# Performance work log

Hardware: AMD Instinct MI355X
Metric: run time of the kernel (lower is better)

Reference implementation:

```python
import jax, jax.numpy as jnp
import numpy as np
import math

B, N, F0, HID, OUT, K = 8, 2048, 128, 64, 16, 10


def setup_inputs() -> dict:
    key = jax.random.key(0)
    ks = jax.random.split(key, 6)
    X = jax.random.normal(ks[0], (B, N, F0), dtype=jnp.float32)
    # Row-stochastic dense 'rescaled Laplacian': spectrum inside unit disk,
    # so K-th order Bernstein polynomial stays numerically stable.
    A = jax.random.uniform(ks[1], (N, N), dtype=jnp.float32)
    L = A / jnp.sum(A, axis=1, keepdims=True)
    W1 = jax.random.normal(ks[2], (F0, HID), dtype=jnp.float32) / np.float32(np.sqrt(F0))
    b1 = jnp.zeros((HID,), dtype=jnp.float32)
    W2 = jax.random.normal(ks[3], (HID, OUT), dtype=jnp.float32) / np.float32(np.sqrt(HID))
    b2 = jnp.zeros((OUT,), dtype=jnp.float32)
    theta = 0.02 * jax.random.normal(ks[4], (K + 1,), dtype=jnp.float32)
    return {"X": X, "L": L, "W1": W1, "b1": b1, "W2": W2, "b2": b2,
            "theta": theta, "dp": 0}


def _bern_filter(Hf, L, theta, binom):
    # g(L) Hf = sum_i theta_i C(K,i) L^i (I-L)^{K-i} Hf
    # Computed by applying L / (I-L) directly to the (B,N,F) features
    # (mathematically identical to forming the NxN basis matrices).
    Lap = lambda Y: jnp.einsum('vw,bwf->bvf', L, Y)
    ys = [Hf]                       # ys[k] = (I-L)^k Hf
    for _ in range(K):
        ys.append(ys[-1] - Lap(ys[-1]))
    a = theta * binom               # (K+1,)
    # Horner in L: r = a_K Hf; r <- L r + a_i (I-L)^{K-i} Hf
    r = a[K] * Hf
    for i in range(K - 1, -1, -1):
        r = Lap(r) + a[i] * ys[K - i]
    return r


def reference(X, L, W1, b1, W2, b2, theta, dp):
    binom = jnp.asarray([math.comb(K, i) for i in range(K + 1)], dtype=X.dtype)
    # dropout with p=dp=0 is identity
    Hf = jax.nn.relu(X @ W1 + b1)          # (B, N, HID)
    Hf = _bern_filter(Hf, L, theta, binom) # (B, N, HID)
    Hg = jnp.mean(Hf, axis=1)              # (B, HID)
    logits = Hg @ W2 + b2                  # (B, OUT)
    return logits
```

## Files before the change

kernel.cpp:

```cpp
#include <hip/hip_runtime.h>

#define NN     2048
#define F0D    128
#define HIDD   64
#define OUTD   16
#define KDEG   10
#define NCHAIN 128
#define COLS   16

typedef unsigned int u32;

#define CTAG(j) (0xC0DE0000u + (u32)(j))
#define HTAG    0xBEEF0001u

static __device__ __forceinline__ u32 ld_flag(const u32* p) {
    return __hip_atomic_load(p, __ATOMIC_RELAXED, __HIP_MEMORY_SCOPE_AGENT);
}
static __device__ __forceinline__ void st_flag(u32* p, u32 v) {
    __hip_atomic_store(p, v, __ATOMIC_RELAXED, __HIP_MEMORY_SCOPE_AGENT);
}
static __device__ __forceinline__ void st_data(float* p, float v) {
    __hip_atomic_store(p, v, __ATOMIC_RELAXED, __HIP_MEMORY_SCOPE_AGENT);
}

__global__ __launch_bounds__(256, 1) void k_fused(
    const float* __restrict__ X, const float* __restrict__ L,
    const float* __restrict__ W1, const float* __restrict__ b1,
    const float* __restrict__ W2, const float* __restrict__ b2,
    const float* __restrict__ theta, float* __restrict__ out,
    float* __restrict__ ws)
{
    float* PB  = ws;
    u32*   FLC = (u32*)(ws + 28672);
    u32*   FLH = (u32*)(ws + 49152);
    float* Hg  = ws + 49280;

    __shared__ union {
        struct { float Lt[NN * COLS]; float redf[4][16]; float cbv[16]; int rdy[16]; } mv;
        struct { float W1t[64][132]; float redm[16][65]; float wv[64]; } hd;
    } sm;

    const int g = blockIdx.x;
    const int t = threadIdx.x;

    if (g < NCHAIN) {
        const int u0 = g * COLS;

        if (t <= KDEG) {
            const float C10[11] = {1,10,45,120,210,252,210,120,45,10,1};
            float acc = 0.f;
            for (int i = 0; i <= t; ++i) {
                int n = KDEG - i, r = t - i;
                long long cm = 1;
                for (int s = 1; s <= r; ++s) cm = cm * (n - r + s) / s;
                float term = theta[i] * C10[i] * (float)cm;
                if ((t - i) & 1) term = -term;
                acc += term;
            }
            sm.mv.cbv[t] = acc;
        }
        if (t < 16) sm.mv.rdy[t] = 0;

        const float4* L4  = (const float4*)L;
        float4*       Lt4 = (float4*)sm.mv.Lt;
        const int qc = t & 3, r0 = t >> 2;
        {
            float4 acc = make_float4(0.f, 0.f, 0.f, 0.f);
            #pragma unroll 8
            for (int i = 0; i < 32; ++i) {
                int v = r0 + 64 * i;
                float4 lv = L4[(size_t)v * (NN / 4) + (u0 >> 2) + qc];
                Lt4[v * 4 + qc] = lv;
                acc.x += lv.x; acc.y += lv.y; acc.z += lv.z; acc.w += lv.w;
            }
            #pragma unroll
            for (int m = 4; m <= 32; m <<= 1) {
                acc.x += __shfl_xor(acc.x, m); acc.y += __shfl_xor(acc.y, m);
                acc.z += __shfl_xor(acc.z, m); acc.w += __shfl_xor(acc.w, m);
            }
            int lane = t & 63, wid = t >> 6;
            if (lane < 4) *(float4*)&sm.mv.redf[wid][lane * 4] = acc;
        }
        __syncthreads();

        float val = 0.f, wacc = 0.f;
        if (t < COLS) {
            float s = sm.mv.redf[0][t] + sm.mv.redf[1][t]
                    + sm.mv.redf[2][t] + sm.mv.redf[3][t];
            val = s; wacc = sm.mv.cbv[0];
            st_data(&PB[u0 + t], s);
        }
        if (t < 64) {
            asm volatile("s_waitcnt vmcnt(0)" ::: "memory");
            if (t == 0) st_flag(FLC + g, CTAG(1));
        }

        for (int j = 2; j <= KDEG; ++j) {
            if (t < 64) {
                const u32* fb = FLC + (size_t)(j - 2) * 128;
                const u32 tag = CTAG(j - 1);
                while (!__all(ld_flag(fb + t) == tag && ld_flag(fb + t + 64) == tag))
                    __builtin_amdgcn_s_sleep(1);
                asm volatile("" ::: "memory");
                if (t == 0) ((volatile int*)sm.mv.rdy)[j] = 1;
            } else {
                volatile int* vr = (volatile int*)sm.mv.rdy;
                while (vr[j] == 0) __builtin_amdgcn_s_sleep(1);
                asm volatile("" ::: "memory");
            }

            const float* psrc = PB + (size_t)(j - 2) * 2048;
            float xv[32];
            #pragma unroll
            for (int k = 0; k < 32; ++k) xv[k] = psrc[r0 + 64 * k];

            float4 a2 = make_float4(0.f, 0.f, 0.f, 0.f);
            #pragma unroll
            for (int k = 0; k < 32; ++k) {
                float4 lv = Lt4[(r0 + 64 * k) * 4 + qc];
                a2.x += lv.x * xv[k]; a2.y += lv.y * xv[k];
                a2.z += lv.z * xv[k]; a2.w += lv.w * xv[k];
            }
            #pragma unroll
            for (int m = 4; m <= 32; m <<= 1) {
                a2.x += __shfl_xor(a2.x, m); a2.y += __shfl_xor(a2.y, m);
                a2.z += __shfl_xor(a2.z, m); a2.w += __shfl_xor(a2.w, m);
            }
            {
                int lane = t & 63, wid = t >> 6;
                if (lane < 4) *(float4*)&sm.mv.redf[wid][lane * 4] = a2;
            }
            __syncthreads();

            if (t < COLS) {
                float s = sm.mv.redf[0][t] + sm.mv.redf[1][t]
                        + sm.mv.redf[2][t] + sm.mv.redf[3][t];
                wacc += sm.mv.cbv[j - 1] * val;
                val = s;
                float outv = (j < KDEG) ? s : (wacc + sm.mv.cbv[KDEG] * s);
                st_data(&PB[(size_t)(j - 1) * 2048 + u0 + t], outv);
            }
            if (t < 64) {
                asm volatile("s_waitcnt vmcnt(0)" ::: "memory");
                if (t == 0) st_flag(FLC + (size_t)(j - 1) * 128 + g, CTAG(j));
            }
        }

        if (g == 0) {
            if (t < 64) {
                for (;;) {
                    int ok = (ld_flag(FLH + t) == HTAG)
                           & (ld_flag(FLH + t + 64) == HTAG);
                    if (__all(ok)) break;
                    __builtin_amdgcn_s_sleep(2);
                }
                asm volatile("" ::: "memory");
            }
            __syncthreads();
            if (t < 128) {
                int o = t & 15, bb = t >> 4;
                float a3 = b2[o];
                #pragma unroll
                for (int h = 0; h < HIDD; ++h)
                    a3 += Hg[bb * 64 + h] * W2[h * 16 + o];
                out[bb * 16 + o] = a3;
            }
        }
        return;
    }

    const int u = g - NCHAIN;
    const int vchunk = u & 31, bA = u >> 5, bB = bA + 4;

    if (t == 0) {
        while (ld_flag(FLC + u) != CTAG(1)) __builtin_amdgcn_s_sleep(2);
    }
    __syncthreads();

    for (int i = t; i < F0D * HIDD; i += 256) {
        int f = i >> 6, h = i & 63;
        sm.hd.W1t[h][f] = W1[i];
    }
    __syncthreads();

    const int hg = t & 15, vg = t >> 4;
    const int vbase = vchunk * 64 + vg * 4;
    const float* XA = X + ((size_t)bA * NN + vbase) * F0D;
    const float* XB = X + ((size_t)bB * NN + vbase) * F0D;
    float accA[4][4] = {}, accB[4][4] = {};
    for (int f = 0; f < F0D; f += 4) {
        float4 xa[4], xb[4];
        #pragma unroll
        for (int i = 0; i < 4; ++i) {
            xa[i] = *(const float4*)(XA + (size_t)i * F0D + f);
            xb[i] = *(const float4*)(XB + (size_t)i * F0D + f);
        }
        #pragma unroll
        for (int jj = 0; jj < 4; ++jj) {
            float4 wr = *(const float4*)(&sm.hd.W1t[hg + 16 * jj][f]);
            #pragma unroll
            for (int i = 0; i < 4; ++i) {
                accA[i][jj] += xa[i].x * wr.x + xa[i].y * wr.y
                             + xa[i].z * wr.z + xa[i].w * wr.w;
                accB[i][jj] += xb[i].x * wr.x + xb[i].y * wr.y
                             + xb[i].z * wr.z + xb[i].w * wr.w;
            }
        }
    }

    if (t < 4) {
        const u32* fp = FLC + (size_t)(KDEG - 1) * 128 + vchunk * 4 + t;
        while (ld_flag(fp) != CTAG(KDEG)) __builtin_amdgcn_s_sleep(2);
        asm volatile("" ::: "memory");
    }
    __syncthreads();
    if (t < 16)
        ((float4*)sm.hd.wv)[t] =
            ((const float4*)(PB + (size_t)(KDEG - 1) * 2048 + vchunk * 64))[t];
    __syncthreads();

    const float inv = 1.0f / (float)NN;
    float hsA[4] = {0.f,0.f,0.f,0.f}, hsB[4] = {0.f,0.f,0.f,0.f};
    #pragma unroll
    for (int i = 0; i < 4; ++i) {
        float we = sm.hd.wv[vg * 4 + i];
        #pragma unroll
        for (int jj = 0; jj < 4; ++jj) {
            float rA = accA[i][jj] + b1[hg + 16 * jj];
            float rB = accB[i][jj] + b1[hg + 16 * jj];
            rA = rA > 0.f ? rA : 0.f;
            rB = rB > 0.f ? rB : 0.f;
            hsA[jj] += rA * we;
            hsB[jj] += rB * we;
        }
    }
    #pragma unroll
    for (int jj = 0; jj < 4; ++jj) sm.hd.redm[vg][hg + 16 * jj] = hsA[jj];
    __syncthreads();
    if (t < 64) {
        float s = 0.f;
        #pragma unroll
        for (int i = 0; i < 16; ++i) s += sm.hd.redm[i][t];
        atomicAdd(&Hg[bA * 64 + t], s * inv);
    }
    __syncthreads();
    #pragma unroll
    for (int jj = 0; jj < 4; ++jj) sm.hd.redm[vg][hg + 16 * jj] = hsB[jj];
    __syncthreads();
    if (t < 64) {
        float s = 0.f;
        #pragma unroll
        for (int i = 0; i < 16; ++i) s += sm.hd.redm[i][t];
        atomicAdd(&Hg[bB * 64 + t], s * inv);
        asm volatile("s_waitcnt vmcnt(0)" ::: "memory");
        if (t == 0) st_flag(FLH + u, HTAG);
    }
}

extern "C" void kernel_launch(void* const* d_in, const int* in_sizes, int n_in,
                              void* d_out, int out_size, void* d_ws, size_t ws_size,
                              hipStream_t stream) {
    const float* X     = (const float*)d_in[0];
    const float* L     = (const float*)d_in[1];
    const float* W1    = (const float*)d_in[2];
    const float* b1    = (const float*)d_in[3];
    const float* W2    = (const float*)d_in[4];
    const float* b2    = (const float*)d_in[5];
    const float* theta = (const float*)d_in[6];
    float* outp = (float*)d_out;
    float* wsp  = (float*)d_ws;

    hipMemsetAsync((char*)d_ws + 49152 * sizeof(float), 0, 2560, stream);

    hipLaunchKernelGGL(k_fused, dim3(256), dim3(256), 0, stream,
                       X, L, W1, b1, W2, b2, theta, outp, wsp);
}
```

Measured before the change: 132.3 us.

## Pad chain flags, double-buffer reductions, and fold W2 projection into head blocks

Each completion flag now sits on its own 64-byte slot to avoid false sharing while many blocks poll. The reduction scratch is double-buffered by step parity, and a second wavefront does the polling. The final step that waited on all head blocks is removed: each head block projects its partial mean through W2 and atomically adds into the zero-initialised output. This removes a serial global wait and an extra pass at the end, but float atomic adds make the summation order nondeterministic.

Result: faster. 118.1 us (-10.8%).

```diff
diff --git a/kernel.cpp b/kernel.cpp
--- a/kernel.cpp
+++ b/kernel.cpp
@@ -11,7 +11,6 @@
 typedef unsigned int u32;
 
 #define CTAG(j) (0xC0DE0000u + (u32)(j))
-#define HTAG    0xBEEF0001u
 
 static __device__ __forceinline__ u32 ld_flag(const u32* p) {
     return __hip_atomic_load(p, __ATOMIC_RELAXED, __HIP_MEMORY_SCOPE_AGENT);
@@ -32,11 +31,10 @@
 {
     float* PB  = ws;
     u32*   FLC = (u32*)(ws + 28672);
-    u32*   FLH = (u32*)(ws + 49152);
-    float* Hg  = ws + 49280;
 
     __shared__ union {
-        struct { float Lt[NN * COLS]; float redf[4][16]; float cbv[16]; int rdy[16]; } mv;
+        struct { float Lt[NN * COLS]; float redf[2][4][16];
+                 float cbv[16]; int rdy[16]; } mv;
         struct { float W1t[64][132]; float redm[16][65]; float wv[64]; } hd;
     } sm;
 
@@ -79,31 +77,35 @@
                 acc.z += __shfl_xor(acc.z, m); acc.w += __shfl_xor(acc.w, m);
             }
             int lane = t & 63, wid = t >> 6;
-            if (lane < 4) *(float4*)&sm.mv.redf[wid][lane * 4] = acc;
+            if (lane < 4) *(float4*)&sm.mv.redf[1][wid][lane * 4] = acc;
         }
         __syncthreads();
 
         float val = 0.f, wacc = 0.f;
         if (t < COLS) {
-            float s = sm.mv.redf[0][t] + sm.mv.redf[1][t]
-                    + sm.mv.redf[2][t] + sm.mv.redf[3][t];
+            float s = sm.mv.redf[1][0][t] + sm.mv.redf[1][1][t]
+                    + sm.mv.redf[1][2][t] + sm.mv.redf[1][3][t];
             val = s; wacc = sm.mv.cbv[0];
             st_data(&PB[u0 + t], s);
         }
         if (t < 64) {
             asm volatile("s_waitcnt vmcnt(0)" ::: "memory");
-            if (t == 0) st_flag(FLC + g, CTAG(1));
+            if (t == 0) st_flag(FLC + g * 16, CTAG(1));
         }
 
         for (int j = 2; j <= KDEG; ++j) {
-            if (t < 64) {
-                const u32* fb = FLC + (size_t)(j - 2) * 128;
+            const int par = j & 1;
+            if ((t >> 6) == 1) {
+                const u32* fb = FLC + (size_t)(j - 2) * 128 * 16;
                 const u32 tag = CTAG(j - 1);
-                while (!__all(ld_flag(fb + t) == tag && ld_flag(fb + t + 64) == tag))
+                const int l = t & 63;
+                while (!__all(ld_flag(fb + l * 16) == tag &&
+                              ld_flag(fb + (l + 64) * 16) == tag))
                     __builtin_amdgcn_s_sleep(1);
                 asm volatile("" ::: "memory");
-                if (t == 0) ((volatile int*)sm.mv.rdy)[j] = 1;
-            } else {
+                if (t == 64) ((volatile int*)sm.mv.rdy)[j] = 1;
+            }
+            {
                 volatile int* vr = (volatile int*)sm.mv.rdy;
                 while (vr[j] == 0) __builtin_amdgcn_s_sleep(1);
                 asm volatile("" ::: "memory");
@@ -128,13 +130,13 @@
             }
             {
                 int lane = t & 63, wid = t >> 6;
-                if (lane < 4) *(float4*)&sm.mv.redf[wid][lane * 4] = a2;
+                if (lane < 4) *(float4*)&sm.mv.redf[par][wid][lane * 4] = a2;
             }
             __syncthreads();
 
             if (t < COLS) {
-                float s = sm.mv.redf[0][t] + sm.mv.redf[1][t]
-                        + sm.mv.redf[2][t] + sm.mv.redf[3][t];
+                float s = sm.mv.redf[par][0][t] + sm.mv.redf[par][1][t]
+                        + sm.mv.redf[par][2][t] + sm.mv.redf[par][3][t];
                 wacc += sm.mv.cbv[j - 1] * val;
                 val = s;
                 float outv = (j < KDEG) ? s : (wacc + sm.mv.cbv[KDEG] * s);
@@ -142,28 +144,8 @@
             }
             if (t < 64) {
                 asm volatile("s_waitcnt vmcnt(0)" ::: "memory");
-                if (t == 0) st_flag(FLC + (size_t)(j - 1) * 128 + g, CTAG(j));
-            }
-        }
-
-        if (g == 0) {
-            if (t < 64) {
-                for (;;) {
-                    int ok = (ld_flag(FLH + t) == HTAG)
-                           & (ld_flag(FLH + t + 64) == HTAG);
-                    if (__all(ok)) break;
-                    __builtin_amdgcn_s_sleep(2);
-                }
-                asm volatile("" ::: "memory");
-            }
-            __syncthreads();
-            if (t < 128) {
-                int o = t & 15, bb = t >> 4;
-                float a3 = b2[o];
-                #pragma unroll
-                for (int h = 0; h < HIDD; ++h)
-                    a3 += Hg[bb * 64 + h] * W2[h * 16 + o];
-                out[bb * 16 + o] = a3;
+                if (t == 0)
+                    st_flag(FLC + ((size_t)(j - 1) * 128 + g) * 16, CTAG(j));
             }
         }
         return;
@@ -173,7 +155,7 @@
     const int vchunk = u & 31, bA = u >> 5, bB = bA + 4;
 
     if (t == 0) {
-        while (ld_flag(FLC + u) != CTAG(1)) __builtin_amdgcn_s_sleep(2);
+        while (ld_flag(FLC + u * 16) != CTAG(1)) __builtin_amdgcn_s_sleep(2);
     }
     __syncthreads();
 
@@ -209,7 +191,7 @@
     }
 
     if (t < 4) {
-        const u32* fp = FLC + (size_t)(KDEG - 1) * 128 + vchunk * 4 + t;
+        const u32* fp = FLC + ((size_t)(KDEG - 1) * 128 + vchunk * 4 + t) * 16;
         while (ld_flag(fp) != CTAG(KDEG)) __builtin_amdgcn_s_sleep(2);
         asm volatile("" ::: "memory");
     }
@@ -234,6 +216,7 @@
             hsB[jj] += rB * we;
         }
     }
+
     #pragma unroll
     for (int jj = 0; jj < 4; ++jj) sm.hd.redm[vg][hg + 16 * jj] = hsA[jj];
     __syncthreads();
@@ -241,9 +224,16 @@
         float s = 0.f;
         #pragma unroll
         for (int i = 0; i < 16; ++i) s += sm.hd.redm[i][t];
-        atomicAdd(&Hg[bA * 64 + t], s * inv);
-    }
-    __syncthreads();
+        sm.hd.wv[t] = s * inv;
+    }
+    __syncthreads();
+    if (t < 16) {
+        float po = 0.f;
+        #pragma unroll
+        for (int h = 0; h < HIDD; ++h) po += sm.hd.wv[h] * W2[h * 16 + t];
+        if (vchunk == 0) po += b2[t];
+        atomicAdd(&out[bA * 16 + t], po);
+    }
     #pragma unroll
     for (int jj = 0; jj < 4; ++jj) sm.hd.redm[vg][hg + 16 * jj] = hsB[jj];
     __syncthreads();
@@ -251,9 +241,15 @@
         float s = 0.f;
         #pragma unroll
         for (int i = 0; i < 16; ++i) s += sm.hd.redm[i][t];
-        atomicAdd(&Hg[bB * 64 + t], s * inv);
-        asm volatile("s_waitcnt vmcnt(0)" ::: "memory");
-        if (t == 0) st_flag(FLH + u, HTAG);
+        sm.hd.wv[t] = s * inv;
+    }
+    __syncthreads();
+    if (t < 16) {
+        float po = 0.f;
+        #pragma unroll
+        for (int h = 0; h < HIDD; ++h) po += sm.hd.wv[h] * W2[h * 16 + t];
+        if (vchunk == 0) po += b2[t];
+        atomicAdd(&out[bB * 16 + t], po);
     }
 }
 
@@ -270,7 +266,7 @@
     float* outp = (float*)d_out;
     float* wsp  = (float*)d_ws;
 
-    hipMemsetAsync((char*)d_ws + 49152 * sizeof(float), 0, 2560, stream);
+    hipMemsetAsync(d_out, 0, out_size, stream);
 
     hipLaunchKernelGGL(k_fused, dim3(256), dim3(256), 0, stream,
                        X, L, W1, b1, W2, b2, theta, outp, wsp);
```
